# Kernel optimization log

Measured on AMD Instinct MI355X. Metric: run time of the kernel, lower is better.

Reference implementation:

```python
import jax, jax.numpy as jnp
import numpy as np

N, E, F_IN = 50000, 800000, 128
H1, C1 = 4, 32          # layer 1: heads, channels (concat -> 128)
H2, C2 = 1, 40          # layer 2: out heads, num_class (mean over heads)
NEG_SLOPE = 0.2


def setup_inputs() -> dict:
    key = jax.random.key(0)
    ks = jax.random.split(key, 10)
    x = jax.random.normal(ks[0], (N, F_IN), dtype=jnp.float32)
    edge_index = jax.random.randint(ks[1], (2, E), 0, N, dtype=jnp.int32)
    s1 = 1.0 / np.sqrt(F_IN)
    s2 = 1.0 / np.sqrt(H1 * C1)
    W1 = jax.random.normal(ks[2], (F_IN, H1 * C1), dtype=jnp.float32) * s1
    att_src1 = jax.random.normal(ks[3], (H1, C1), dtype=jnp.float32) * s1
    att_dst1 = jax.random.normal(ks[4], (H1, C1), dtype=jnp.float32) * s1
    b1 = jnp.zeros((H1 * C1,), dtype=jnp.float32)
    W2 = jax.random.normal(ks[5], (H1 * C1, H2 * C2), dtype=jnp.float32) * s2
    att_src2 = jax.random.normal(ks[6], (H2, C2), dtype=jnp.float32) * s2
    att_dst2 = jax.random.normal(ks[7], (H2, C2), dtype=jnp.float32) * s2
    b2 = jnp.zeros((C2,), dtype=jnp.float32)
    return {"x": x, "edge_index": edge_index, "W1": W1, "att_src1": att_src1,
            "att_dst1": att_dst1, "b1": b1, "W2": W2, "att_src2": att_src2,
            "att_dst2": att_dst2, "b2": b2}


def _gat_layer(x, src, dst, W, a_src, a_dst, b, concat):
    # PyG GATConv (eval): linear -> per-head attention logits on edges ->
    # segment-softmax over each destination's in-edges -> scatter-aggregate.
    n = x.shape[0]
    Hh, C = a_src.shape
    h = (x @ W).reshape(n, Hh, C)                       # [N,H,C]
    al_s = jnp.sum(h * a_src, axis=-1)                  # [N,H]
    al_d = jnp.sum(h * a_dst, axis=-1)                  # [N,H]
    alpha = jax.nn.leaky_relu(al_s[src] + al_d[dst], NEG_SLOPE)  # [E,H]
    m = jax.lax.stop_gradient(jax.ops.segment_max(alpha, dst, num_segments=n))
    e = jnp.exp(alpha - m[dst])
    denom = jax.ops.segment_sum(e, dst, num_segments=n)
    a = e / (denom[dst] + 1e-16)                        # [E,H]
    out = jax.ops.segment_sum(h[src] * a[..., None], dst, num_segments=n)
    out = out.reshape(n, Hh * C) if concat else out.mean(axis=1)
    return out + b


def reference(x, edge_index, W1, att_src1, att_dst1, b1, W2, att_src2, att_dst2, b2):
    n = x.shape[0]
    loop = jnp.arange(n, dtype=edge_index.dtype)        # GATConv add_self_loops=True
    src = jnp.concatenate([edge_index[0], loop])
    dst = jnp.concatenate([edge_index[1], loop])
    h = _gat_layer(x, src, dst, W1, att_src1, att_dst1, b1, concat=True)
    h = jax.nn.elu(h)
    out = _gat_layer(h, src, dst, W2, att_src2, att_dst2, b2, concat=False)
    return out
```

## Files before the change

### kernel.cpp

```cpp
#include <hip/hip_runtime.h>
#include <hip/hip_bf16.h>
#include <hip/hip_fp16.h>
#include <math.h>

constexpr int N_NODES = 50000;
constexpr int E_EDGES = 800000;
constexpr float NEG_SLOPE = 0.2f;
constexpr int CAP = 64;
constexpr int G1_BLOCKS   = (N_NODES + 63) / 64;
constexpr int LINK_CHUNKS = (E_EDGES + 2047) / 2048;
constexpr int LINK_BLOCKS = LINK_CHUNKS * 8;
constexpr int RANGE_SZ    = N_NODES / 8;

typedef _Float16 half8 __attribute__((ext_vector_type(8)));
typedef _Float16 half2v __attribute__((ext_vector_type(2)));
typedef float    floatx4 __attribute__((ext_vector_type(4)));

static inline int cdiv(long long a, int b) { return (int)((a + b - 1) / b); }

__device__ inline float leaky(float a) { return a > 0.f ? a : NEG_SLOPE * a; }
__device__ inline unsigned pack2h(float a, float b) {
    union { _Float16 h[2]; unsigned u; } p;
    p.h[0] = (_Float16)a; p.h[1] = (_Float16)b; return p.u;
}
__device__ inline float2 unp2h(unsigned u) {
    __half2 hh = *reinterpret_cast<__half2*>(&u);
    return __half22float2(hh);
}
__device__ inline float sel4(const float4& v, int h) {
    float a = (h & 2) ? v.z : v.x;
    float b = (h & 2) ? v.w : v.y;
    return (h & 1) ? b : a;
}

__global__ __launch_bounds__(256) void prep_kernel(const float* __restrict__ W1,
                                                   const float* __restrict__ W2,
                                                   int* __restrict__ deg,
                                                   _Float16* __restrict__ w1t,
                                                   _Float16* __restrict__ w2t) {
    int b = blockIdx.x, t = threadIdx.x;
    if (b < 196) {
        int i = b * 256 + t;
        if (i < N_NODES) deg[i] = 0;
        return;
    }
    if (b < 196 + 64) {
        int idx = (b - 196) * 256 + t;
        int k = idx >> 7, c = idx & 127;
        w1t[c * 128 + k] = (_Float16)W1[k * 128 + c];
        return;
    }
    {
        int idx = (b - 260) * 256 + t;
        int k = idx / 40, c = idx - k * 40;
        w2t[c * 128 + k] = (_Float16)W2[k * 40 + c];
    }
}

__global__ __launch_bounds__(256, 8) void gemm1_link_kernel(const float* __restrict__ x,
                                                            const _Float16* __restrict__ w1t,
                                                            const float* __restrict__ as1,
                                                            const float* __restrict__ ad1,
                                                            unsigned short* __restrict__ h1h,
                                                            float* __restrict__ als,
                                                            float* __restrict__ ald,
                                                            const int* __restrict__ ei,
                                                            int* __restrict__ deg,
                                                            unsigned short* __restrict__ csr16) {
    __shared__ _Float16 xS[64 * 136];
    __shared__ float asld[128], adld[128];
    int t = threadIdx.x;

    if (blockIdx.x >= G1_BLOCKS) {
        int lb    = blockIdx.x - G1_BLOCKS;
        int range = lb & 7;
        int chunk = lb >> 3;
        int e0    = chunk * 2048 + t * 8;
        if (e0 < E_EDGES) {
            int4 sa = *(const int4*)&ei[e0];
            int4 sb = *(const int4*)&ei[e0 + 4];
            int4 da = *(const int4*)&ei[E_EDGES + e0];
            int4 db = *(const int4*)&ei[E_EDGES + e0 + 4];
            int ss[8] = { sa.x, sa.y, sa.z, sa.w, sb.x, sb.y, sb.z, sb.w };
            int dd[8] = { da.x, da.y, da.z, da.w, db.x, db.y, db.z, db.w };
            int dlo = range * RANGE_SZ, dhi = dlo + RANGE_SZ;
            #pragma unroll
            for (int j = 0; j < 8; ++j) {
                if (dd[j] >= dlo && dd[j] < dhi) {
                    int slot = atomicAdd(&deg[dd[j]], 1) + 1;
                    if (slot < CAP) csr16[dd[j] * CAP + slot] = (unsigned short)ss[j];
                }
            }
        }
        return;
    }

    int row0 = blockIdx.x * 64;
    if (t < 128) { asld[t] = as1[t]; adld[t] = ad1[t]; }
    #pragma unroll
    for (int i = 0; i < 8; ++i) {
        int fi = i * 256 + t;
        int r = fi >> 5, c4 = (fi & 31) * 4;
        int gr = row0 + r;
        float4 v = make_float4(0.f, 0.f, 0.f, 0.f);
        if (gr < N_NODES) v = *(const float4*)&x[(size_t)gr * 128 + c4];
        union { _Float16 h[4]; uint2 u; } pk;
        pk.h[0] = (_Float16)v.x; pk.h[1] = (_Float16)v.y;
        pk.h[2] = (_Float16)v.z; pk.h[3] = (_Float16)v.w;
        *(uint2*)&xS[r * 136 + c4] = pk.u;
    }
    __syncthreads();

    int w = t >> 6, lane = t & 63, quad = lane >> 4, l16 = lane & 15;
    floatx4 z = {0.f, 0.f, 0.f, 0.f};
    floatx4 c[4][2];
    #pragma unroll
    for (int rt = 0; rt < 4; ++rt) { c[rt][0] = z; c[rt][1] = z; }

    const _Float16* wt0 = w1t + (size_t)(w * 32 + l16) * 128;
    const _Float16* wt1 = wt0 + 16 * 128;
    #pragma unroll
    for (int ks = 0; ks < 4; ++ks) {
        int kg = ks * 32 + quad * 8;
        half8 b0 = *(const half8*)&wt0[kg];
        half8 b1 = *(const half8*)&wt1[kg];
        #pragma unroll
        for (int rt = 0; rt < 4; ++rt) {
            half8 a = *(const half8*)&xS[(rt * 16 + l16) * 136 + kg];
            c[rt][0] = __builtin_amdgcn_mfma_f32_16x16x32_f16(a, b0, c[rt][0], 0, 0, 0);
            c[rt][1] = __builtin_amdgcn_mfma_f32_16x16x32_f16(a, b1, c[rt][1], 0, 0, 0);
        }
    }
    __syncthreads();
    _Float16* cbuf = xS;
    #pragma unroll
    for (int rt = 0; rt < 4; ++rt)
        #pragma unroll
        for (int ctl = 0; ctl < 2; ++ctl)
            #pragma unroll
            for (int reg = 0; reg < 4; ++reg)
                cbuf[(rt * 16 + quad * 4 + reg) * 136 + (w * 32 + ctl * 16 + l16)]
                    = (_Float16)c[rt][ctl][reg];
    __syncthreads();
    int r = t >> 2, hq = t & 3;
    int n = row0 + r;
    if (n < N_NODES) {
        if (hq == 0) csr16[n * CAP] = (unsigned short)n;
        float ps = 0.f, pd = 0.f;
        #pragma unroll
        for (int i = 0; i < 4; ++i) {
            uint4 uv = *(uint4*)&cbuf[r * 136 + hq * 32 + i * 8];
            *(uint4*)&h1h[(size_t)n * 128 + hq * 32 + i * 8] = uv;
            union { uint4 u; _Float16 h[8]; } cv; cv.u = uv;
            #pragma unroll
            for (int k = 0; k < 8; ++k) {
                float v = (float)cv.h[k];
                ps += v * asld[hq * 32 + i * 8 + k];
                pd += v * adld[hq * 32 + i * 8 + k];
            }
        }
        als[n * 4 + hq] = ps;
        ald[n * 4 + hq] = pd;
    }
}

__global__ __launch_bounds__(1024, 8) void agg1_gemm2_kernel(const int* __restrict__ deg_,
                                                             const unsigned short* __restrict__ csr16,
                                                             const float* __restrict__ als,
                                                             const float4* __restrict__ ald4,
                                                             const unsigned short* __restrict__ h1h,
                                                             const float* __restrict__ b1,
                                                             const _Float16* __restrict__ w2t,
                                                             const float* __restrict__ as2,
                                                             const float* __restrict__ ad2,
                                                             unsigned short* __restrict__ h2h,
                                                             float* __restrict__ als2,
                                                             float* __restrict__ ald2) {
    __shared__ _Float16 aS[64 * 136];
    __shared__ float asld[40], adld[40];
    int t = threadIdx.x;
    int wv   = t >> 6;
    int lane = t & 63;
    if (t < 40) { asld[t] = as2[t]; adld[t] = ad2[t]; }
    int row0 = blockIdx.x * 64;
    int half = lane >> 5;
    int l    = lane & 31;
    int myhead = l >> 3;
    int we   = lane & 15;
    int wh   = lane >> 4;

    for (int jd = 0; jd < 4; ++jd) {
        int tr = wv * 4 + jd;
        int d  = row0 + tr;
        if (d < N_NODES) {
            int dg   = min(deg_[d] + 1, CAP);
            int base = d * CAP;
            float4 aldd = ald4[d];
            float d_hw = sel4(aldd, wh);
            float sm = 0.f;
            float acc[4] = {0.f, 0.f, 0.f, 0.f};
            int sfirst = (int)csr16[base];
            #pragma unroll 2
            for (int j = 0; j < dg; j += 16) {
                int s_w = (int)csr16[base + j + we];
                float av = als[s_w * 4 + wh];
                float wgt = (j + we < dg) ? __expf(leaky(av + d_hw)) : 0.f;
                uint4 blkA = *(const uint4*)&csr16[base + j];
                uint4 blkB = *(const uint4*)&csr16[base + j + 8];
                unsigned bw[8] = { blkA.x, blkA.y, blkA.z, blkA.w,
                                   blkB.x, blkB.y, blkB.z, blkB.w };
                int ss[8];
                #pragma unroll
                for (int p = 0; p < 8; ++p) {
                    unsigned b = __builtin_amdgcn_readfirstlane(bw[p]);
                    int e0 = (int)(b & 0xffff), e1 = (int)(b >> 16);
                    int mys = half ? e1 : e0;
                    if (j + 2 * p + half >= dg) mys = sfirst;
                    ss[p] = mys;
                }
                uint2 hv[8];
                #pragma unroll
                for (int p = 0; p < 8; ++p)
                    hv[p] = *(const uint2*)(h1h + ((size_t)ss[p] << 7) + 4 * l);
                float ww[8];
                #pragma unroll
                for (int p = 0; p < 8; ++p) {
                    ww[p] = __shfl(wgt, 16 * myhead + 2 * p + half);
                    sm += ww[p];
                }
                half2v hacc0 = { (_Float16)0.f, (_Float16)0.f };
                half2v hacc1 = { (_Float16)0.f, (_Float16)0.f };
                #pragma unroll
                for (int p = 0; p < 8; ++p) {
                    half2v v0 = *reinterpret_cast<half2v*>(&hv[p].x);
                    half2v v1 = *reinterpret_cast<half2v*>(&hv[p].y);
                    _Float16 hw = (_Float16)ww[p];
                    half2v hwv = { hw, hw };
                    hacc0 += v0 * hwv;
                    hacc1 += v1 * hwv;
                }
                acc[0] += (float)hacc0[0]; acc[1] += (float)hacc0[1];
                acc[2] += (float)hacc1[0]; acc[3] += (float)hacc1[1];
            }
            sm += __shfl_xor(sm, 32);
            #pragma unroll
            for (int k = 0; k < 4; ++k) acc[k] += __shfl_xor(acc[k], 32);
            if (half == 0) {
                float inv = 1.f / (sm + 1e-16f);
                float v[4];
                #pragma unroll
                for (int k = 0; k < 4; ++k) {
                    v[k] = acc[k] * inv + b1[4 * l + k];
                    v[k] = v[k] > 0.f ? v[k] : __expf(v[k]) - 1.f;
                }
                uint2 o;
                o.x = pack2h(v[0], v[1]);
                o.y = pack2h(v[2], v[3]);
                *(uint2*)&aS[tr * 136 + 4 * l] = o;
            }
        } else if (half == 0) {
            *(uint2*)&aS[tr * 136 + 4 * l] = make_uint2(0u, 0u);
        }
    }
    __syncthreads();

    if (wv < 4) {
        int w = wv, quad = lane >> 4, l16 = lane & 15;
        floatx4 z = {0.f, 0.f, 0.f, 0.f};
        floatx4 c0 = z, c1 = z, c2 = z;
        int n2 = (l16 < 8) ? 32 + l16 : 39;
        const _Float16* wb0 = w2t + (size_t)l16 * 128;
        const _Float16* wb1 = w2t + (size_t)(16 + l16) * 128;
        const _Float16* wb2 = w2t + (size_t)n2 * 128;
        #pragma unroll
        for (int ks = 0; ks < 4; ++ks) {
            int kg = ks * 32 + quad * 8;
            half8 b0 = *(const half8*)&wb0[kg];
            half8 b1 = *(const half8*)&wb1[kg];
            half8 b2 = *(const half8*)&wb2[kg];
            half8 a  = *(const half8*)&aS[(w * 16 + l16) * 136 + kg];
            c0 = __builtin_amdgcn_mfma_f32_16x16x32_f16(a, b0, c0, 0, 0, 0);
            c1 = __builtin_amdgcn_mfma_f32_16x16x32_f16(a, b1, c1, 0, 0, 0);
            c2 = __builtin_amdgcn_mfma_f32_16x16x32_f16(a, b2, c2, 0, 0, 0);
        }
        #pragma unroll
        for (int reg = 0; reg < 4; ++reg) {
            int rr = (w * 16 + quad * 4 + reg) * 136;
            aS[rr + l16]      = (_Float16)c0[reg];
            aS[rr + 16 + l16] = (_Float16)c1[reg];
            aS[rr + 32 + l16] = (_Float16)c2[reg];
        }
    }
    __syncthreads();

    if (t < 320) {
        int r = t / 5, s = t - r * 5;
        int n = row0 + r;
        if (n < N_NODES) {
            uint4 v = *(uint4*)&aS[r * 136 + s * 8];
            *(uint4*)&h2h[(size_t)n * 40 + s * 8] = v;
        }
    }
    if (t < 256) {
        int r = t >> 2, q = t & 3;
        int n = row0 + r;
        float ps = 0.f, pd = 0.f;
        #pragma unroll
        for (int i = 0; i < 10; ++i) {
            int cc = q * 10 + i;
            float v = (float)aS[r * 136 + cc];
            ps += v * asld[cc]; pd += v * adld[cc];
        }
        ps += __shfl_xor(ps, 1); ps += __shfl_xor(ps, 2);
        pd += __shfl_xor(pd, 1); pd += __shfl_xor(pd, 2);
        if (q == 0 && n < N_NODES) { als2[n] = ps; ald2[n] = pd; }
    }
}

__global__ __launch_bounds__(256) void agg2_kernel(const int* __restrict__ deg_,
                                                   const unsigned short* __restrict__ csr16,
                                                   const float* __restrict__ als,
                                                   const float* __restrict__ ald,
                                                   const unsigned short* __restrict__ h2h,
                                                   const float* __restrict__ b2,
                                                   float* __restrict__ out) {
    int wv   = threadIdx.x >> 6;
    int lane = threadIdx.x & 63;
    int d    = blockIdx.x * 4 + wv;
    int dg   = min(deg_[d] + 1, CAP);
    int base = d * CAP;
    float aldd = ald[d];

    int slot = lane / 20;
    int idx  = lane - slot * 20;
    int sfirst = (int)csr16[base];
    float sm = 0.f, acc0 = 0.f, acc1 = 0.f;
    if (lane < 60) {
        #pragma unroll 2
        for (int jb = 0; jb < dg; jb += 12) {
            int ss[4]; unsigned hv[4]; float ww[4];
            #pragma unroll
            for (int i = 0; i < 4; ++i) {
                int jj = jb + slot + 3 * i;
                ss[i] = (jj < dg) ? (int)csr16[base + jj] : sfirst;
            }
            #pragma unroll
            for (int i = 0; i < 4; ++i)
                hv[i] = *(const unsigned*)(h2h + (size_t)ss[i] * 40 + 2 * idx);
            #pragma unroll
            for (int i = 0; i < 4; ++i) {
                int jj = jb + slot + 3 * i;
                float w = __expf(leaky(als[ss[i]] + aldd));
                ww[i] = (jj < dg) ? w : 0.f;
            }
            #pragma unroll
            for (int i = 0; i < 4; ++i) {
                float2 f = unp2h(hv[i]);
                acc0 += f.x * ww[i]; acc1 += f.y * ww[i]; sm += ww[i];
            }
        }
    }
    float s1 = __shfl(sm,   idx + 20), s2 = __shfl(sm,   idx + 40);
    float t0 = __shfl(acc0, idx + 20), t1 = __shfl(acc0, idx + 40);
    float u0 = __shfl(acc1, idx + 20), u1 = __shfl(acc1, idx + 40);
    sm += s1 + s2; acc0 += t0 + t1; acc1 += u0 + u1;
    if (lane < 20) {
        float inv = 1.f / (sm + 1e-16f);
        float2 o = make_float2(acc0 * inv + b2[2 * lane], acc1 * inv + b2[2 * lane + 1]);
        *(float2*)&out[(size_t)d * 40 + 2 * lane] = o;
    }
}

constexpr size_t OFF_H1H    = 0;
constexpr size_t OFF_H2H    = 3200000;
constexpr size_t OFF_ALS1   = 6400000;
constexpr size_t OFF_ALD1   = 6600000;
constexpr size_t OFF_W1T    = 6800000;
constexpr size_t OFF_W2T    = 6808192;
constexpr size_t OFF_DEG    = 6860000;
constexpr size_t OFF_CSRF   = 6920000;
constexpr size_t OFF_ALS2   = 8520000;
constexpr size_t OFF_ALD2   = 8570000;
constexpr size_t WS_FLOATS  = 10120000;

extern "C" void kernel_launch(void* const* d_in, const int* in_sizes, int n_in,
                              void* d_out, int out_size, void* d_ws, size_t ws_size,
                              hipStream_t stream) {
    const float* x   = (const float*)d_in[0];
    const int*   ei  = (const int*)  d_in[1];
    const float* W1  = (const float*)d_in[2];
    const float* as1 = (const float*)d_in[3];
    const float* ad1 = (const float*)d_in[4];
    const float* b1  = (const float*)d_in[5];
    const float* W2  = (const float*)d_in[6];
    const float* as2 = (const float*)d_in[7];
    const float* ad2 = (const float*)d_in[8];
    const float* b2  = (const float*)d_in[9];
    float* out = (float*)d_out;

    if (ws_size < WS_FLOATS * sizeof(float)) return;

    float* ws = (float*)d_ws;
    unsigned short* h1h   = (unsigned short*)(ws + OFF_H1H);
    unsigned short* h2h   = (unsigned short*)(ws + OFF_H2H);
    float* als1    = ws + OFF_ALS1;
    float* ald1    = ws + OFF_ALD1;
    float* als2    = ws + OFF_ALS2;
    float* ald2    = ws + OFF_ALD2;
    _Float16* w1t  = (_Float16*)(ws + OFF_W1T);
    _Float16* w2t  = (_Float16*)(ws + OFF_W2T);
    int*   deg     = (int*)(ws + OFF_DEG);
    unsigned short* csr16 = (unsigned short*)(ws + OFF_CSRF);

    prep_kernel<<<280, 256, 0, stream>>>(W1, W2, deg, w1t, w2t);
    gemm1_link_kernel<<<G1_BLOCKS + LINK_BLOCKS, 256, 0, stream>>>(
        x, w1t, as1, ad1, h1h, als1, ald1, ei, deg, csr16);

    agg1_gemm2_kernel<<<cdiv(N_NODES, 64), 1024, 0, stream>>>(
        deg, csr16, als1, (const float4*)ald1, h1h, b1,
        w2t, as2, ad2, h2h, als2, ald2);

    agg2_kernel<<<N_NODES / 4, 256, 0, stream>>>(deg, csr16, als2, ald2, h2h, b2, out);
}
```

Before: 210.5 us.

## Shrink agg1_gemm2 blocks to 4 nodes and replace MFMA GEMM2 with fdot2

The fused aggregation and second-layer GEMM kernel now runs one 256-thread block per 4 destination nodes instead of 1024-thread blocks each handling 64 nodes, with one wave per node. The small 4x128x40 GEMM is done with scalar fdot2 dot products instead of MFMA tiles. The aim is finer-grained load balancing, more blocks and less shared memory per block. The trade-off is heavier per-block W2 reads and fewer threads busy during the GEMM phase. The edge-linking pass also now loads source indices lazily, only for edges that fall in the block's destination range.

```diff
diff --git a/kernel.cpp b/kernel.cpp
--- a/kernel.cpp
+++ b/kernel.cpp
@@ -32,6 +32,16 @@
     float b = (h & 2) ? v.w : v.y;
     return (h & 1) ? b : a;
 }
+
+#if __has_builtin(__builtin_amdgcn_fdot2)
+__device__ inline float dot2f(half2v a, half2v b, float c) {
+    return __builtin_amdgcn_fdot2(a, b, c, false);
+}
+#else
+__device__ inline float dot2f(half2v a, half2v b, float c) {
+    return c + (float)a[0] * (float)b[0] + (float)a[1] * (float)b[1];
+}
+#endif
 
 __global__ __launch_bounds__(256) void prep_kernel(const float* __restrict__ W1,
                                                    const float* __restrict__ W2,
@@ -77,18 +87,16 @@
         int chunk = lb >> 3;
         int e0    = chunk * 2048 + t * 8;
         if (e0 < E_EDGES) {
-            int4 sa = *(const int4*)&ei[e0];
-            int4 sb = *(const int4*)&ei[e0 + 4];
             int4 da = *(const int4*)&ei[E_EDGES + e0];
             int4 db = *(const int4*)&ei[E_EDGES + e0 + 4];
-            int ss[8] = { sa.x, sa.y, sa.z, sa.w, sb.x, sb.y, sb.z, sb.w };
             int dd[8] = { da.x, da.y, da.z, da.w, db.x, db.y, db.z, db.w };
             int dlo = range * RANGE_SZ, dhi = dlo + RANGE_SZ;
             #pragma unroll
             for (int j = 0; j < 8; ++j) {
                 if (dd[j] >= dlo && dd[j] < dhi) {
                     int slot = atomicAdd(&deg[dd[j]], 1) + 1;
-                    if (slot < CAP) csr16[dd[j] * CAP + slot] = (unsigned short)ss[j];
+                    if (slot < CAP)
+                        csr16[dd[j] * CAP + slot] = (unsigned short)ei[e0 + j];
                 }
             }
         }
@@ -164,156 +172,137 @@
     }
 }
 
-__global__ __launch_bounds__(1024, 8) void agg1_gemm2_kernel(const int* __restrict__ deg_,
-                                                             const unsigned short* __restrict__ csr16,
-                                                             const float* __restrict__ als,
-                                                             const float4* __restrict__ ald4,
-                                                             const unsigned short* __restrict__ h1h,
-                                                             const float* __restrict__ b1,
-                                                             const _Float16* __restrict__ w2t,
-                                                             const float* __restrict__ as2,
-                                                             const float* __restrict__ ad2,
-                                                             unsigned short* __restrict__ h2h,
-                                                             float* __restrict__ als2,
-                                                             float* __restrict__ ald2) {
-    __shared__ _Float16 aS[64 * 136];
+__global__ __launch_bounds__(256) void agg1_gemm2_kernel(const int* __restrict__ deg_,
+                                                         const unsigned short* __restrict__ csr16,
+                                                         const float* __restrict__ als,
+                                                         const float4* __restrict__ ald4,
+                                                         const unsigned short* __restrict__ h1h,
+                                                         const float* __restrict__ b1,
+                                                         const _Float16* __restrict__ w2t,
+                                                         const float* __restrict__ as2,
+                                                         const float* __restrict__ ad2,
+                                                         unsigned short* __restrict__ h2h,
+                                                         float* __restrict__ als2,
+                                                         float* __restrict__ ald2) {
+    __shared__ _Float16 o1S[4][128];
+    __shared__ _Float16 h2S[4][40];
     __shared__ float asld[40], adld[40];
     int t = threadIdx.x;
     int wv   = t >> 6;
     int lane = t & 63;
     if (t < 40) { asld[t] = as2[t]; adld[t] = ad2[t]; }
-    int row0 = blockIdx.x * 64;
     int half = lane >> 5;
     int l    = lane & 31;
     int myhead = l >> 3;
     int we   = lane & 15;
     int wh   = lane >> 4;
-
-    for (int jd = 0; jd < 4; ++jd) {
-        int tr = wv * 4 + jd;
-        int d  = row0 + tr;
-        if (d < N_NODES) {
-            int dg   = min(deg_[d] + 1, CAP);
-            int base = d * CAP;
-            float4 aldd = ald4[d];
-            float d_hw = sel4(aldd, wh);
-            float sm = 0.f;
-            float acc[4] = {0.f, 0.f, 0.f, 0.f};
-            int sfirst = (int)csr16[base];
-            #pragma unroll 2
-            for (int j = 0; j < dg; j += 16) {
-                int s_w = (int)csr16[base + j + we];
-                float av = als[s_w * 4 + wh];
-                float wgt = (j + we < dg) ? __expf(leaky(av + d_hw)) : 0.f;
-                uint4 blkA = *(const uint4*)&csr16[base + j];
-                uint4 blkB = *(const uint4*)&csr16[base + j + 8];
-                unsigned bw[8] = { blkA.x, blkA.y, blkA.z, blkA.w,
-                                   blkB.x, blkB.y, blkB.z, blkB.w };
-                int ss[8];
-                #pragma unroll
-                for (int p = 0; p < 8; ++p) {
-                    unsigned b = __builtin_amdgcn_readfirstlane(bw[p]);
-                    int e0 = (int)(b & 0xffff), e1 = (int)(b >> 16);
-                    int mys = half ? e1 : e0;
-                    if (j + 2 * p + half >= dg) mys = sfirst;
-                    ss[p] = mys;
-                }
-                uint2 hv[8];
-                #pragma unroll
-                for (int p = 0; p < 8; ++p)
-                    hv[p] = *(const uint2*)(h1h + ((size_t)ss[p] << 7) + 4 * l);
-                float ww[8];
-                #pragma unroll
-                for (int p = 0; p < 8; ++p) {
-                    ww[p] = __shfl(wgt, 16 * myhead + 2 * p + half);
-                    sm += ww[p];
-                }
-                half2v hacc0 = { (_Float16)0.f, (_Float16)0.f };
-                half2v hacc1 = { (_Float16)0.f, (_Float16)0.f };
-                #pragma unroll
-                for (int p = 0; p < 8; ++p) {
-                    half2v v0 = *reinterpret_cast<half2v*>(&hv[p].x);
-                    half2v v1 = *reinterpret_cast<half2v*>(&hv[p].y);
-                    _Float16 hw = (_Float16)ww[p];
-                    half2v hwv = { hw, hw };
-                    hacc0 += v0 * hwv;
-                    hacc1 += v1 * hwv;
-                }
-                acc[0] += (float)hacc0[0]; acc[1] += (float)hacc0[1];
-                acc[2] += (float)hacc1[0]; acc[3] += (float)hacc1[1];
-            }
-            sm += __shfl_xor(sm, 32);
-            #pragma unroll
-            for (int k = 0; k < 4; ++k) acc[k] += __shfl_xor(acc[k], 32);
-            if (half == 0) {
-                float inv = 1.f / (sm + 1e-16f);
-                float v[4];
-                #pragma unroll
-                for (int k = 0; k < 4; ++k) {
-                    v[k] = acc[k] * inv + b1[4 * l + k];
-                    v[k] = v[k] > 0.f ? v[k] : __expf(v[k]) - 1.f;
-                }
-                uint2 o;
-                o.x = pack2h(v[0], v[1]);
-                o.y = pack2h(v[2], v[3]);
-                *(uint2*)&aS[tr * 136 + 4 * l] = o;
-            }
-        } else if (half == 0) {
-            *(uint2*)&aS[tr * 136 + 4 * l] = make_uint2(0u, 0u);
-        }
+    int d    = blockIdx.x * 4 + wv;
+    int dg   = min(deg_[d] + 1, CAP);
+    int base = d * CAP;
+    float4 aldd = ald4[d];
+    float d_hw = sel4(aldd, wh);
+
+    float sm = 0.f;
+    float acc[4] = {0.f, 0.f, 0.f, 0.f};
+    int sfirst = (int)csr16[base];
+    #pragma unroll 2
+    for (int j = 0; j < dg; j += 16) {
+        int s_w = (int)csr16[base + j + we];
+        float av = als[s_w * 4 + wh];
+        float wgt = (j + we < dg) ? __expf(leaky(av + d_hw)) : 0.f;
+        uint4 blkA = *(const uint4*)&csr16[base + j];
+        uint4 blkB = *(const uint4*)&csr16[base + j + 8];
+        unsigned bw[8] = { blkA.x, blkA.y, blkA.z, blkA.w,
+                           blkB.x, blkB.y, blkB.z, blkB.w };
+        int ss[8];
+        #pragma unroll
+        for (int p = 0; p < 8; ++p) {
+            unsigned b = __builtin_amdgcn_readfirstlane(bw[p]);
+            int e0 = (int)(b & 0xffff), e1 = (int)(b >> 16);
+            int mys = half ? e1 : e0;
+            if (j + 2 * p + half >= dg) mys = sfirst;
+            ss[p] = mys;
+        }
+        uint2 hv[8];
+        #pragma unroll
+        for (int p = 0; p < 8; ++p)
+            hv[p] = *(const uint2*)(h1h + ((size_t)ss[p] << 7) + 4 * l);
+        float ww[8];
+        #pragma unroll
+        for (int p = 0; p < 8; ++p) {
+            ww[p] = __shfl(wgt, 16 * myhead + 2 * p + half);
+            sm += ww[p];
+        }
+        half2v hacc0 = { (_Float16)0.f, (_Float16)0.f };
+        half2v hacc1 = { (_Float16)0.f, (_Float16)0.f };
+        #pragma unroll
+        for (int p = 0; p < 8; ++p) {
+            half2v v0 = *reinterpret_cast<half2v*>(&hv[p].x);
+            half2v v1 = *reinterpret_cast<half2v*>(&hv[p].y);
+            _Float16 hw = (_Float16)ww[p];
+            half2v hwv = { hw, hw };
+            hacc0 += v0 * hwv;
+            hacc1 += v1 * hwv;
+        }
+        acc[0] += (float)hacc0[0]; acc[1] += (float)hacc0[1];
+        acc[2] += (float)hacc1[0]; acc[3] += (float)hacc1[1];
+    }
+    sm += __shfl_xor(sm, 32);
+    #pragma unroll
+    for (int k = 0; k < 4; ++k) acc[k] += __shfl_xor(acc[k], 32);
+    if (half == 0) {
+        float inv = 1.f / (sm + 1e-16f);
+        float v[4];
+        #pragma unroll
+        for (int k = 0; k < 4; ++k) {
+            v[k] = acc[k] * inv + b1[4 * l + k];
+            v[k] = v[k] > 0.f ? v[k] : __expf(v[k]) - 1.f;
+        }
+        uint2 o;
+        o.x = pack2h(v[0], v[1]);
+        o.y = pack2h(v[2], v[3]);
+        *(uint2*)&o1S[wv][4 * l] = o;
     }
     __syncthreads();
 
-    if (wv < 4) {
-        int w = wv, quad = lane >> 4, l16 = lane & 15;
-        floatx4 z = {0.f, 0.f, 0.f, 0.f};
-        floatx4 c0 = z, c1 = z, c2 = z;
-        int n2 = (l16 < 8) ? 32 + l16 : 39;
-        const _Float16* wb0 = w2t + (size_t)l16 * 128;
-        const _Float16* wb1 = w2t + (size_t)(16 + l16) * 128;
-        const _Float16* wb2 = w2t + (size_t)n2 * 128;
-        #pragma unroll
-        for (int ks = 0; ks < 4; ++ks) {
-            int kg = ks * 32 + quad * 8;
-            half8 b0 = *(const half8*)&wb0[kg];
-            half8 b1 = *(const half8*)&wb1[kg];
-            half8 b2 = *(const half8*)&wb2[kg];
-            half8 a  = *(const half8*)&aS[(w * 16 + l16) * 136 + kg];
-            c0 = __builtin_amdgcn_mfma_f32_16x16x32_f16(a, b0, c0, 0, 0, 0);
-            c1 = __builtin_amdgcn_mfma_f32_16x16x32_f16(a, b1, c1, 0, 0, 0);
-            c2 = __builtin_amdgcn_mfma_f32_16x16x32_f16(a, b2, c2, 0, 0, 0);
-        }
-        #pragma unroll
-        for (int reg = 0; reg < 4; ++reg) {
-            int rr = (w * 16 + quad * 4 + reg) * 136;
-            aS[rr + l16]      = (_Float16)c0[reg];
-            aS[rr + 16 + l16] = (_Float16)c1[reg];
-            aS[rr + 32 + l16] = (_Float16)c2[reg];
-        }
+    if (t < 160) {
+        int r = t / 40, cc = t - r * 40;
+        const half8* xr = (const half8*)o1S[r];
+        const half8* wr = (const half8*)(w2t + (size_t)cc * 128);
+        float h2c = 0.f;
+        #pragma unroll
+        for (int kk = 0; kk < 16; ++kk) {
+            half8 a = xr[kk], b = wr[kk];
+            #pragma unroll
+            for (int q = 0; q < 4; ++q) {
+                half2v a2 = { a[2 * q], a[2 * q + 1] };
+                half2v b2 = { b[2 * q], b[2 * q + 1] };
+                h2c = dot2f(a2, b2, h2c);
+            }
+        }
+        h2S[r][cc] = (_Float16)h2c;
     }
     __syncthreads();
 
-    if (t < 320) {
+    if (t < 20) {
         int r = t / 5, s = t - r * 5;
-        int n = row0 + r;
-        if (n < N_NODES) {
-            uint4 v = *(uint4*)&aS[r * 136 + s * 8];
-            *(uint4*)&h2h[(size_t)n * 40 + s * 8] = v;
-        }
-    }
-    if (t < 256) {
+        *(uint4*)&h2h[(size_t)(blockIdx.x * 4 + r) * 40 + s * 8] = *(uint4*)&h2S[r][s * 8];
+    }
+    if (t < 16) {
         int r = t >> 2, q = t & 3;
-        int n = row0 + r;
         float ps = 0.f, pd = 0.f;
         #pragma unroll
         for (int i = 0; i < 10; ++i) {
             int cc = q * 10 + i;
-            float v = (float)aS[r * 136 + cc];
+            float v = (float)h2S[r][cc];
             ps += v * asld[cc]; pd += v * adld[cc];
         }
         ps += __shfl_xor(ps, 1); ps += __shfl_xor(ps, 2);
         pd += __shfl_xor(pd, 1); pd += __shfl_xor(pd, 2);
-        if (q == 0 && n < N_NODES) { als2[n] = ps; ald2[n] = pd; }
+        if (q == 0) {
+            int n = blockIdx.x * 4 + r;
+            als2[n] = ps; ald2[n] = pd;
+        }
     }
 }
 
@@ -416,7 +405,7 @@
     gemm1_link_kernel<<<G1_BLOCKS + LINK_BLOCKS, 256, 0, stream>>>(
         x, w1t, as1, ad1, h1h, als1, ald1, ei, deg, csr16);
 
-    agg1_gemm2_kernel<<<cdiv(N_NODES, 64), 1024, 0, stream>>>(
+    agg1_gemm2_kernel<<<N_NODES / 4, 256, 0, stream>>>(
         deg, csr16, als1, (const float4*)ald1, h1h, b1,
         w2t, as2, ad2, h2h, als2, ald2);
 
```

Measured after the change: 245.0 us. 1.16x slower.
